# Kernel tuning notes

Hardware: AMD Instinct MI355X
Metric: run time of the kernel (lower is better)

Reference implementation:

```python
import jax, jax.numpy as jnp
import numpy as np

B, C, N, K, COUT = 4, 64, 8192, 16, 64
EPS = 1e-5  # BatchNorm1d default eps


def setup_inputs() -> dict:
    key = jax.random.key(0)
    k1, k2, k3 = jax.random.split(key, 3)
    x = jax.random.normal(k1, (B, C, N), dtype=jnp.float32)
    coords = jax.random.normal(k2, (B, 3, N), dtype=jnp.float32)
    # Linear(2C -> COUT) params
    W = jax.random.normal(k3, (2 * C, COUT), dtype=jnp.float32) * (1.0 / np.sqrt(2 * C))
    b = jnp.zeros((COUT,), dtype=jnp.float32)
    # BatchNorm1d affine params (train-mode batch stats, as in torch default)
    gamma = jnp.ones((COUT,), dtype=jnp.float32)
    beta = jnp.zeros((COUT,), dtype=jnp.float32)
    return {"x": x, "coords": coords, "W": W, "b": b, "gamma": gamma, "beta": beta}


def reference(x, coords, W, b, gamma, beta):
    k = min(K, max(N - 1, 1))
    # --- kNN in coordinate space (squared distances give same ordering as cdist) ---
    ct = jnp.swapaxes(coords, 1, 2)                      # (B, N, 3)
    sq = jnp.sum(ct * ct, axis=-1)                       # (B, N)
    d2 = sq[:, :, None] + sq[:, None, :] - 2.0 * jnp.einsum('bnd,bmd->bnm', ct, ct)
    _, idx = jax.lax.top_k(-d2, k + 1)                   # smallest k+1 distances
    idx = idx[:, :, 1:]                                  # drop self -> (B, N, k)
    # --- gather neighbor features ---
    xt = jnp.swapaxes(x, 1, 2)                           # (B, N, C)
    nb = jax.vmap(lambda f, i: f[i])(xt, idx)            # (B, N, k, C)
    center = jnp.broadcast_to(xt[:, :, None, :], nb.shape)
    edge = jnp.concatenate([center, nb - center], axis=-1)  # (B, N, k, 2C)
    # --- edge MLP: Linear -> BatchNorm1d (batch stats) -> ReLU ---
    h = jnp.einsum('bnkc,cd->bnkd', edge, W) + b         # (B, N, k, COUT)
    mean = jnp.mean(h, axis=(0, 1, 2))
    var = jnp.var(h, axis=(0, 1, 2))
    h = (h - mean) * jax.lax.rsqrt(var + EPS) * gamma + beta
    h = jax.nn.relu(h)
    # --- max-pool over k neighbors ---
    out = jnp.max(h, axis=2)                             # (B, N, COUT)
    return jnp.swapaxes(out, 1, 2)                       # (B, COUT, N)
```

## Files before the change

kernel.cpp:

```cpp
#include <hip/hip_runtime.h>


#define Bn 4
#define Nn 8192
#define Gc 32
#define CS 32896
#define Hc 0.375f

typedef unsigned long long ull;

__device__ __forceinline__ int cellof(float v) {
  int i = (int)floorf((v + 6.0f) * (1.0f / Hc));
  return min(Gc - 1, max(0, i));
}

__global__ __launch_bounds__(256) void transpose_kernel(const float* __restrict__ x,
                                                        const float* __restrict__ coords,
                                                        float* __restrict__ xt,
                                                        float4* __restrict__ cpack) {
  __shared__ float tile[64][65];
  int bid = blockIdx.x;
  int b = bid >> 7;
  int n0 = (bid & 127) << 6;
  int tx = threadIdx.x & 63;
  int ty = threadIdx.x >> 6;
  for (int c = ty; c < 64; c += 4)
    tile[tx][c] = x[((size_t)b * 64 + c) * Nn + n0 + tx];
  if (ty == 0) {
    int n = n0 + tx;
    const float* cb = coords + (size_t)b * 3 * Nn;
    float cx = cb[n], cy = cb[Nn + n], cz = cb[2 * Nn + n];
    float cs = __fadd_rn(__fadd_rn(__fmul_rn(cx, cx), __fmul_rn(cy, cy)),
                         __fmul_rn(cz, cz));
    cpack[(size_t)b * Nn + n] = make_float4(cx, cy, cz, cs);
  }
  __syncthreads();
  for (int r = ty; r < 64; r += 4)
    xt[((size_t)b * Nn + n0 + r) * 64 + tx] = tile[r][tx];
}

__global__ __launch_bounds__(256) void hist_kernel(const float4* __restrict__ cpack,
                                                   unsigned* __restrict__ cells,
                                                   unsigned* __restrict__ cstart) {
  int n = blockIdx.x * 256 + threadIdx.x;
  float4 c = cpack[n];
  unsigned cell = ((unsigned)cellof(c.z) * Gc + cellof(c.y)) * Gc + cellof(c.x);
  cells[n] = cell;
  atomicAdd(&cstart[(unsigned)(n >> 13) * CS + cell], 1u);
}

__global__ __launch_bounds__(256) void scanA_kernel(unsigned* __restrict__ cstart,
                                                    unsigned* __restrict__ partials) {
  __shared__ unsigned sums[256];
  int bid = blockIdx.x, b = bid >> 4, ch = bid & 15, t = threadIdx.x;
  unsigned* base = cstart + (size_t)b * CS + ch * 2048 + t * 8;
  unsigned v[8], p = 0;
#pragma unroll
  for (int j = 0; j < 8; ++j) { unsigned c = base[j]; v[j] = p; p += c; }
  sums[t] = p;
  __syncthreads();
  for (int off = 1; off < 256; off <<= 1) {
    unsigned u = (t >= off) ? sums[t - off] : 0u;
    __syncthreads();
    sums[t] += u;
    __syncthreads();
  }
  unsigned excl = sums[t] - p;
#pragma unroll
  for (int j = 0; j < 8; ++j) base[j] = v[j] + excl;
  if (t == 255) partials[bid] = sums[255];
}

__global__ __launch_bounds__(256) void scanC_kernel(unsigned* __restrict__ cstart,
                                                    unsigned* __restrict__ cursor,
                                                    const unsigned* __restrict__ partials) {
  int bid = blockIdx.x, b = bid >> 4, ch = bid & 15, t = threadIdx.x;
  unsigned off = 0;
  for (int k = 0; k < ch; ++k) off += partials[b * 16 + k];
  size_t o = (size_t)b * CS + ch * 2048 + t * 8;
#pragma unroll
  for (int j = 0; j < 8; ++j) {
    unsigned val = cstart[o + j] + off;
    cstart[o + j] = val;
    cursor[o + j] = val;
  }
}

__global__ __launch_bounds__(256) void scatter_kernel(const float4* __restrict__ cpack,
                                                      const unsigned* __restrict__ cells,
                                                      unsigned* __restrict__ cursor,
                                                      float4* __restrict__ spos4,
                                                      unsigned* __restrict__ sidx) {
  int n = blockIdx.x * 256 + threadIdx.x;
  int b = n >> 13;
  unsigned slot = atomicAdd(&cursor[(size_t)b * CS + cells[n]], 1u);
  spos4[(size_t)b * Nn + slot] = cpack[n];
  sidx[(size_t)b * Nn + slot] = (unsigned)(n & 8191);
}

__global__ __launch_bounds__(256) void bbox_kernel(const float4* __restrict__ spos4,
                                                   float4* __restrict__ bbox) {
  __shared__ float4 smn[256], smx[256];
  int blk = blockIdx.x;
  int t = threadIdx.x;
  const float4* sp = spos4 + (size_t)(blk >> 4) * Nn + (blk & 15) * 512;
  float4 a = sp[t], c = sp[t + 256];
  smn[t] = make_float4(fminf(a.x, c.x), fminf(a.y, c.y), fminf(a.z, c.z), 0.f);
  smx[t] = make_float4(fmaxf(a.x, c.x), fmaxf(a.y, c.y), fmaxf(a.z, c.z), 0.f);
  __syncthreads();
  for (int off = 128; off > 0; off >>= 1) {
    if (t < off) {
      float4 n2 = smn[t + off], x2 = smx[t + off], n1 = smn[t], x1 = smx[t];
      smn[t] = make_float4(fminf(n1.x, n2.x), fminf(n1.y, n2.y), fminf(n1.z, n2.z), 0.f);
      smx[t] = make_float4(fmaxf(x1.x, x2.x), fmaxf(x1.y, x2.y), fmaxf(x1.z, x2.z), 0.f);
    }
    __syncthreads();
  }
  if (t == 0) { bbox[blk * 2] = smn[0]; bbox[blk * 2 + 1] = smx[0]; }
}

#define RMAX(kv) do {                                         \
    ull _kk = (kv);                                           \
    _Pragma("unroll")                                         \
    for (int _u = 0; _u < 16; ++_u)                           \
      ad[_u] = (ad[_u] == thr) ? _kk : ad[_u];                \
    ull _t0 = ad[0] > ad[1] ? ad[0] : ad[1];                  \
    ull _t1 = ad[2] > ad[3] ? ad[2] : ad[3];                  \
    ull _t2 = ad[4] > ad[5] ? ad[4] : ad[5];                  \
    ull _t3 = ad[6] > ad[7] ? ad[6] : ad[7];                  \
    ull _t4 = ad[8] > ad[9] ? ad[8] : ad[9];                  \
    ull _t5 = ad[10] > ad[11] ? ad[10] : ad[11];              \
    ull _t6 = ad[12] > ad[13] ? ad[12] : ad[13];              \
    ull _t7 = ad[14] > ad[15] ? ad[14] : ad[15];              \
    ull _u0 = _t0 > _t1 ? _t0 : _t1;                          \
    ull _u1 = _t2 > _t3 ? _t2 : _t3;                          \
    ull _u2 = _t4 > _t5 ? _t4 : _t5;                          \
    ull _u3 = _t6 > _t7 ? _t6 : _t7;                          \
    ull _v0 = _u0 > _u1 ? _u0 : _u1;                          \
    ull _v1 = _u2 > _u3 ? _u2 : _u3;                          \
    thr = _v0 > _v1 ? _v0 : _v1;                              \
  } while (0)

#define SINS(kv) do {                                         \
    ull _kk = (kv);                                           \
    if (_kk < nad[15]) {                                      \
      bool _ci = true;                                        \
      _Pragma("unroll")                                       \
      for (int _u = 15; _u >= 1; --_u) {                      \
        bool _cm = _kk < nad[_u - 1];                         \
        nad[_u] = _ci ? (_cm ? nad[_u - 1] : _kk) : nad[_u];  \
        _ci = _cm;                                            \
      }                                                       \
      nad[0] = _ci ? _kk : nad[0];                            \
    }                                                         \
  } while (0)

__global__ __launch_bounds__(256) void knn_kernel(const float4* __restrict__ spos4,
                                                  const unsigned* __restrict__ sidx,
                                                  const float4* __restrict__ bbox,
                                                  int* __restrict__ knn) {
  __shared__ __align__(16) ull mk[7 * 16 * 32];
  __shared__ unsigned sthr[32];

  int bid = blockIdx.x;
  int b = bid >> 8;
  int grp = bid & 255;
  int tid = threadIdx.x;
  int lane = tid & 63;
  int l32 = lane & 31;
  int s = tid >> 6;
  int ss = (s << 1) | (lane >> 5);
  int qslot = grp * 32 + l32;

  const float4* sp = spos4 + (size_t)b * Nn;
  const unsigned* sx = sidx + (size_t)b * Nn;

  float4 qc = sp[qslot];
  unsigned qg = sx[qslot];
  float qs = qc.w;
  float qx2 = 2.f * qc.x, qy2 = 2.f * qc.y, qz2 = 2.f * qc.z;

  if (tid < 32) sthr[tid] = 0xFFFFFFFFu;
  __syncthreads();

  ull ad[16];
#pragma unroll
  for (int i = 0; i < 16; ++i) ad[i] = 0xFFFFFFFF00000000ull | (unsigned)i;
  ull thr = 0xFFFFFFFF0000000Full;
  unsigned thr_hi = 0xFFFFFFFFu;

  int m0 = grp >> 4;
  int visited = 0;
  for (int step = 0; step < 32 && visited < 16; ++step) {
    int d = (step + 1) >> 1;
    int m = (step & 1) ? (m0 + d) : (m0 - d);
    if (m < 0 || m >= 16) continue;
    ++visited;

    float4 bmn = bbox[(b * 16 + m) * 2];
    float4 bmx = bbox[(b * 16 + m) * 2 + 1];
    float ddx = fmaxf(fmaxf(bmn.x - qc.x, qc.x - bmx.x), 0.f);
    float ddy = fmaxf(fmaxf(bmn.y - qc.y, qc.y - bmx.y), 0.f);
    float ddz = fmaxf(fmaxf(bmn.z - qc.z, qc.z - bmx.z), 0.f);
    float dmin2 = ddx * ddx + ddy * ddy + ddz * ddz;
    unsigned shu = sthr[l32];
    int skipl = (dmin2 > __uint_as_float(shu) + 1e-3f) ? 1 : 0;
    if (__all(skipl)) continue;

    int loc0 = m * 512 + ss * 32;
#pragma unroll
    for (int half = 0; half < 2; ++half) {
      int base = loc0 + half * 256;
      const float4* cpb = sp + base;
      const unsigned* sxb = sx + base;
      unsigned sh = sthr[l32];
      thr_hi = sh < thr_hi ? sh : thr_hi;
      unsigned mask = 0;
#pragma unroll 8
      for (int j = 0; j < 32; ++j) {
        float4 c4 = cpb[j];
        float dot2 = __fadd_rn(__fadd_rn(__fmul_rn(qx2, c4.x), __fmul_rn(qy2, c4.y)),
                               __fmul_rn(qz2, c4.z));
        float d2 = __fsub_rn(__fadd_rn(qs, c4.w), dot2);
        mask |= (__float_as_uint(d2) <= thr_hi) ? (1u << j) : 0u;
      }
      unsigned sj = (unsigned)(qslot - base);
      if (sj < 32u) mask &= ~(1u << sj);
      while (__any(mask)) {
        if (mask) {
          int j = __ffs(mask) - 1;
          mask &= (mask - 1);
          float4 c4 = cpb[j];
          float dot2 = __fadd_rn(__fadd_rn(__fmul_rn(qx2, c4.x), __fmul_rn(qy2, c4.y)),
                                 __fmul_rn(qz2, c4.z));
          float d2 = __fsub_rn(__fadd_rn(qs, c4.w), dot2);
          ull key = ((ull)__float_as_uint(d2) << 32) | sxb[j];
          if (key < thr) RMAX(key);
        }
      }
      unsigned lh = (unsigned)(thr >> 32);
      thr_hi = lh < thr_hi ? lh : thr_hi;
      atomicMin(&sthr[l32], lh);
    }
  }

  __syncthreads();
  if (lane >= 32) {
    int row = 2 * s;
#pragma unroll
    for (int i = 0; i < 16; ++i) mk[(row * 16 + i) * 32 + l32] = ad[i];
  } else if (s > 0) {
    int row = 2 * s - 1;
#pragma unroll
    for (int i = 0; i < 16; ++i) mk[(row * 16 + i) * 32 + l32] = ad[i];
  }
  __syncthreads();
  if (s == 0 && lane < 32) {
    ull nad[16];
#pragma unroll
    for (int i = 0; i < 16; ++i) nad[i] = ~0ull;
#pragma unroll
    for (int i = 0; i < 16; ++i) SINS(ad[i]);
    for (int t = 0; t < 7 * 16; ++t) SINS(mk[t * 32 + l32]);
    int* op = knn + (size_t)(b * Nn + (int)qg) * 16;
#pragma unroll
    for (int i = 0; i < 16; ++i) op[i] = (int)(nad[i] & 0xFFFFFFFFull);
  }
}

__global__ __launch_bounds__(256, 2) void edge_kernel(
    const float* __restrict__ xt, const int* __restrict__ knn,
    const float* __restrict__ W, const float* __restrict__ bias,
    float* __restrict__ mnb, float* __restrict__ mxb,
    float* __restrict__ ps1, float* __restrict__ ps2) {
  __shared__ float dlds[4][16][64];
  __shared__ float clds[4][64];
  __shared__ float r1[4][64], r2[4][64];

  int tid = threadIdx.x;
  int l = tid & 63;
  int w = tid >> 6;

  float w1[64], w2[64];
#pragma unroll
  for (int c = 0; c < 64; ++c) {
    w1[c] = W[c * 64 + l];
    w2[c] = W[(64 + c) * 64 + l];
  }
  float bl = bias[l];
  float s1 = 0.f, s2 = 0.f;

  int wid = blockIdx.x * 4 + w;
  int nw = gridDim.x * 4;
  for (int p = wid; p < Bn * Nn; p += nw) {
    int bb = p >> 13;
    const float* xb = xt + (size_t)bb * Nn * 64;
    float ctr = xt[(size_t)p * 64 + l];
    clds[w][l] = ctr;
    const int* ip = knn + (size_t)p * 16;
#pragma unroll
    for (int j = 0; j < 16; ++j) {
      int nj = ip[j];
      dlds[w][j][l] = xb[(size_t)nj * 64 + l] - ctr;
    }
    __syncthreads();

    const float4* cv = (const float4*)clds[w];
    float cc = bl;
#pragma unroll
    for (int c = 0; c < 16; ++c) {
      float4 v = cv[c];
      cc = fmaf(v.w, w1[4 * c + 3], fmaf(v.z, w1[4 * c + 2],
           fmaf(v.y, w1[4 * c + 1], fmaf(v.x, w1[4 * c + 0], cc))));
    }

    float mn = 3.0e38f, mx = -3.0e38f;
#pragma unroll
    for (int k = 0; k < 16; ++k) {
      const float4* dv = (const float4*)dlds[w][k];
      float h = cc;
#pragma unroll
      for (int c = 0; c < 16; ++c) {
        float4 v = dv[c];
        h = fmaf(v.w, w2[4 * c + 3], fmaf(v.z, w2[4 * c + 2],
            fmaf(v.y, w2[4 * c + 1], fmaf(v.x, w2[4 * c + 0], h))));
      }
      mn = fminf(mn, h);
      mx = fmaxf(mx, h);
      s1 += h;
      s2 = fmaf(h, h, s2);
    }
    mnb[(size_t)p * 64 + l] = mn;
    mxb[(size_t)p * 64 + l] = mx;
    __syncthreads();
  }

  r1[w][l] = s1; r2[w][l] = s2;
  __syncthreads();
  if (w == 0) {
    float a = r1[0][l] + r1[1][l] + r1[2][l] + r1[3][l];
    float c2 = r2[0][l] + r2[1][l] + r2[2][l] + r2[3][l];
    ps1[blockIdx.x * 64 + l] = a;
    ps2[blockIdx.x * 64 + l] = c2;
  }
}

__global__ __launch_bounds__(256) void stats_kernel(const float* __restrict__ ps1,
                                                    const float* __restrict__ ps2,
                                                    float* __restrict__ stats) {
  __shared__ float r1[4][64], r2[4][64];
  int c = threadIdx.x & 63, g = threadIdx.x >> 6;
  float a = 0.f, b2 = 0.f;
  for (int i = g; i < 512; i += 4) { a += ps1[i * 64 + c]; b2 += ps2[i * 64 + c]; }
  r1[g][c] = a; r2[g][c] = b2;
  __syncthreads();
  if (g == 0) {
    float s1 = r1[0][c] + r1[1][c] + r1[2][c] + r1[3][c];
    float s2 = r2[0][c] + r2[1][c] + r2[2][c] + r2[3][c];
    const float invM = 1.f / 524288.f;
    float mean = s1 * invM;
    float var = s2 * invM - mean * mean;
    stats[c] = mean;
    stats[64 + c] = var;
  }
}

__global__ __launch_bounds__(256) void final_kernel(
    const float* __restrict__ mnb, const float* __restrict__ mxb,
    const float* __restrict__ stats, const float* __restrict__ gamma,
    const float* __restrict__ beta, float* __restrict__ out) {
  __shared__ float tile[64][65];
  int bid = blockIdx.x;
  int b = bid >> 7;
  int n0 = (bid & 127) << 6;
  int tx = threadIdx.x & 63, ty = threadIdx.x >> 6;
  float mean = stats[tx], var = stats[64 + tx];
  float sc = gamma[tx] * rsqrtf(var + 1e-5f);
  float sh = fmaf(-mean, sc, beta[tx]);
  for (int r = ty; r < 64; r += 4) {
    size_t off = ((size_t)(b * Nn + n0 + r)) * 64 + tx;
    float lo = fmaf(mnb[off], sc, sh);
    float hi = fmaf(mxb[off], sc, sh);
    tile[tx][r] = fmaxf(fmaxf(hi, lo), 0.f);
  }
  __syncthreads();
  for (int r = ty; r < 64; r += 4)
    out[((size_t)b * 64 + r) * Nn + n0 + tx] = tile[r][tx];
}

extern "C" void kernel_launch(void* const* d_in, const int* in_sizes, int n_in,
                              void* d_out, int out_size, void* d_ws, size_t ws_size,
                              hipStream_t stream) {
  const float* x      = (const float*)d_in[0];
  const float* coords = (const float*)d_in[1];
  const float* W      = (const float*)d_in[2];
  const float* bias   = (const float*)d_in[3];
  const float* gamma  = (const float*)d_in[4];
  const float* beta   = (const float*)d_in[5];
  float* out = (float*)d_out;

  char* ws = (char*)d_ws;
  float*    xt       = (float*)ws;
  int*      knn      = (int*)(ws + 8388608);
  float*    mnb      = (float*)(ws + 10485760);
  float4*   cpack    = (float4*)(ws + 10485760);
  float*    mxb      = (float*)(ws + 18874368);
  float4*   spos4    = (float4*)(ws + 18874368);
  unsigned* cstart   = (unsigned*)(ws + 19398656);
  unsigned* cursor   = (unsigned*)(ws + 19924992);
  unsigned* cells    = (unsigned*)(ws + 20451328);
  unsigned* partials = (unsigned*)(ws + 20582400);
  unsigned* sidx     = (unsigned*)(ws + 20582656);
  float4*   bbox     = (float4*)(ws + 20713728);
  float*    ps1      = (float*)(ws + 27262976);
  float*    ps2      = (float*)(ws + 27394048);
  float*    stats    = (float*)(ws + 27525120);

  transpose_kernel<<<dim3(512), dim3(256), 0, stream>>>(x, coords, xt, cpack);
  hipMemsetAsync(cstart, 0, (size_t)4 * CS * 4, stream);
  hist_kernel<<<dim3(128), dim3(256), 0, stream>>>(cpack, cells, cstart);
  scanA_kernel<<<dim3(64), dim3(256), 0, stream>>>(cstart, partials);
  scanC_kernel<<<dim3(64), dim3(256), 0, stream>>>(cstart, cursor, partials);
  scatter_kernel<<<dim3(128), dim3(256), 0, stream>>>(cpack, cells, cursor, spos4, sidx);
  bbox_kernel<<<dim3(64), dim3(256), 0, stream>>>(spos4, bbox);
  knn_kernel<<<dim3(1024), dim3(256), 0, stream>>>(spos4, sidx, bbox, knn);
  edge_kernel<<<dim3(512), dim3(256), 0, stream>>>(xt, knn, W, bias, mnb, mxb, ps1, ps2);
  stats_kernel<<<dim3(1), dim3(256), 0, stream>>>(ps1, ps2, stats);
  final_kernel<<<dim3(512), dim3(256), 0, stream>>>(mnb, mxb, stats, gamma, beta, out);
}
```

Measured before the change: 569.0 us.

## Add per-32-point sub-block bounding boxes for finer kNN candidate pruning

Adds a small kernel that computes axis-aligned bounding boxes for each run of 32 sorted points. The kNN kernel uses these to skip 32-point chunks whose box lies beyond the current per-query distance threshold, in addition to the existing 512-point block test. The per-wave work split changes from two 32-point halves to four 16-point pieces per sub-block. This adds a kernel launch, extra box loads and more wave-wide votes, in exchange for fewer distance evaluations and fewer candidate insertions.

Result: slower. 612.8 us (+7.7%).

```diff
diff --git a/kernel.cpp b/kernel.cpp
--- a/kernel.cpp
+++ b/kernel.cpp
@@ -117,6 +117,28 @@
     __syncthreads();
   }
   if (t == 0) { bbox[blk * 2] = smn[0]; bbox[blk * 2 + 1] = smx[0]; }
+}
+
+__global__ __launch_bounds__(64) void wbox_kernel(const float4* __restrict__ spos4,
+                                                  float4* __restrict__ wbox) {
+  int w = blockIdx.x;
+  int t = threadIdx.x & 31;
+  float4 c = spos4[(size_t)(w >> 8) * Nn + (w & 255) * 32 + t];
+  float mnx = c.x, mny = c.y, mnz = c.z;
+  float mxx = c.x, mxy = c.y, mxz = c.z;
+#pragma unroll
+  for (int m = 16; m >= 1; m >>= 1) {
+    mnx = fminf(mnx, __shfl_xor(mnx, m));
+    mny = fminf(mny, __shfl_xor(mny, m));
+    mnz = fminf(mnz, __shfl_xor(mnz, m));
+    mxx = fmaxf(mxx, __shfl_xor(mxx, m));
+    mxy = fmaxf(mxy, __shfl_xor(mxy, m));
+    mxz = fmaxf(mxz, __shfl_xor(mxz, m));
+  }
+  if (threadIdx.x == 0) {
+    wbox[w * 2]     = make_float4(mnx, mny, mnz, 0.f);
+    wbox[w * 2 + 1] = make_float4(mxx, mxy, mxz, 0.f);
+  }
 }
 
 #define RMAX(kv) do {                                         \
@@ -158,6 +180,7 @@
 __global__ __launch_bounds__(256) void knn_kernel(const float4* __restrict__ spos4,
                                                   const unsigned* __restrict__ sidx,
                                                   const float4* __restrict__ bbox,
+                                                  const float4* __restrict__ wbox,
                                                   int* __restrict__ knn) {
   __shared__ __align__(16) ull mk[7 * 16 * 32];
   __shared__ unsigned sthr[32];
@@ -168,8 +191,8 @@
   int tid = threadIdx.x;
   int lane = tid & 63;
   int l32 = lane & 31;
+  int hh = lane >> 5;
   int s = tid >> 6;
-  int ss = (s << 1) | (lane >> 5);
   int qslot = grp * 32 + l32;
 
   const float4* sp = spos4 + (size_t)b * Nn;
@@ -197,27 +220,40 @@
     if (m < 0 || m >= 16) continue;
     ++visited;
 
-    float4 bmn = bbox[(b * 16 + m) * 2];
-    float4 bmx = bbox[(b * 16 + m) * 2 + 1];
-    float ddx = fmaxf(fmaxf(bmn.x - qc.x, qc.x - bmx.x), 0.f);
-    float ddy = fmaxf(fmaxf(bmn.y - qc.y, qc.y - bmx.y), 0.f);
-    float ddz = fmaxf(fmaxf(bmn.z - qc.z, qc.z - bmx.z), 0.f);
-    float dmin2 = ddx * ddx + ddy * ddy + ddz * ddz;
-    unsigned shu = sthr[l32];
-    int skipl = (dmin2 > __uint_as_float(shu) + 1e-3f) ? 1 : 0;
-    if (__all(skipl)) continue;
-
-    int loc0 = m * 512 + ss * 32;
-#pragma unroll
-    for (int half = 0; half < 2; ++half) {
-      int base = loc0 + half * 256;
+    {
+      unsigned sh = sthr[l32];
+      thr_hi = sh < thr_hi ? sh : thr_hi;
+      float4 bmn = bbox[(b * 16 + m) * 2];
+      float4 bmx = bbox[(b * 16 + m) * 2 + 1];
+      float ddx = fmaxf(fmaxf(bmn.x - qc.x, qc.x - bmx.x), 0.f);
+      float ddy = fmaxf(fmaxf(bmn.y - qc.y, qc.y - bmx.y), 0.f);
+      float ddz = fmaxf(fmaxf(bmn.z - qc.z, qc.z - bmx.z), 0.f);
+      float dmin2 = ddx * ddx + ddy * ddy + ddz * ddz;
+      int skipl = (dmin2 > __uint_as_float(thr_hi) + 1e-3f) ? 1 : 0;
+      if (__all(skipl)) continue;
+    }
+
+    int mbase = m * 512;
+#pragma unroll
+    for (int wi = 0; wi < 4; ++wi) {
+      int widx = s + wi * 4;
+      const float4* wb = wbox + (size_t)((b * 256 + (m << 4) + widx) << 1);
+      float4 wmn = wb[0], wmx = wb[1];
+      float ex = fmaxf(fmaxf(wmn.x - qc.x, qc.x - wmx.x), 0.f);
+      float ey = fmaxf(fmaxf(wmn.y - qc.y, qc.y - wmx.y), 0.f);
+      float ez = fmaxf(fmaxf(wmn.z - qc.z, qc.z - wmx.z), 0.f);
+      float wd2 = ex * ex + ey * ey + ez * ez;
+      unsigned sh = sthr[l32];
+      thr_hi = sh < thr_hi ? sh : thr_hi;
+      int wskip = (wd2 > __uint_as_float(thr_hi) + 1e-3f) ? 1 : 0;
+      if (__all(wskip)) continue;
+
+      int base = mbase + widx * 32 + hh * 16;
       const float4* cpb = sp + base;
       const unsigned* sxb = sx + base;
-      unsigned sh = sthr[l32];
-      thr_hi = sh < thr_hi ? sh : thr_hi;
       unsigned mask = 0;
-#pragma unroll 8
-      for (int j = 0; j < 32; ++j) {
+#pragma unroll
+      for (int j = 0; j < 16; ++j) {
         float4 c4 = cpb[j];
         float dot2 = __fadd_rn(__fadd_rn(__fmul_rn(qx2, c4.x), __fmul_rn(qy2, c4.y)),
                                __fmul_rn(qz2, c4.z));
@@ -225,7 +261,7 @@
         mask |= (__float_as_uint(d2) <= thr_hi) ? (1u << j) : 0u;
       }
       unsigned sj = (unsigned)(qslot - base);
-      if (sj < 32u) mask &= ~(1u << sj);
+      if (sj < 16u) mask &= ~(1u << sj);
       while (__any(mask)) {
         if (mask) {
           int j = __ffs(mask) - 1;
@@ -412,6 +448,7 @@
   unsigned* partials = (unsigned*)(ws + 20582400);
   unsigned* sidx     = (unsigned*)(ws + 20582656);
   float4*   bbox     = (float4*)(ws + 20713728);
+  float4*   wbox     = (float4*)(ws + 20715776);
   float*    ps1      = (float*)(ws + 27262976);
   float*    ps2      = (float*)(ws + 27394048);
   float*    stats    = (float*)(ws + 27525120);
@@ -423,7 +460,8 @@
   scanC_kernel<<<dim3(64), dim3(256), 0, stream>>>(cstart, cursor, partials);
   scatter_kernel<<<dim3(128), dim3(256), 0, stream>>>(cpack, cells, cursor, spos4, sidx);
   bbox_kernel<<<dim3(64), dim3(256), 0, stream>>>(spos4, bbox);
-  knn_kernel<<<dim3(1024), dim3(256), 0, stream>>>(spos4, sidx, bbox, knn);
+  wbox_kernel<<<dim3(1024), dim3(64), 0, stream>>>(spos4, wbox);
+  knn_kernel<<<dim3(1024), dim3(256), 0, stream>>>(spos4, sidx, bbox, wbox, knn);
   edge_kernel<<<dim3(512), dim3(256), 0, stream>>>(xt, knn, W, bias, mnb, mxb, ps1, ps2);
   stats_kernel<<<dim3(1), dim3(256), 0, stream>>>(ps1, ps2, stats);
   final_kernel<<<dim3(512), dim3(256), 0, stream>>>(mnb, mxb, stats, gamma, beta, out);
```
